# Optimization experiments

Measured on AMD Instinct MI355X. Metric: run time of the kernel, lower is better.

Reference implementation:

```python
import jax, jax.numpy as jnp
import numpy as np
import math

NUM_LEVELS = 16
LEVEL_DIM = 2
BASE_RES = 16
MAX_RES = 2048
HASHMAP_SIZE = 1 << 19  # 2**log2_hashmap_size
B, N = 4, 262144


def setup_inputs() -> dict:
    key = jax.random.key(0)
    k1, k2 = jax.random.split(key)
    x = jax.random.uniform(k1, (B, N, 3), dtype=jnp.float32)  # coords in [0,1]
    # per-level hash tables, init uniform(-1e-4, 1e-4) as in the torch module
    embeddings = jax.random.uniform(
        k2, (NUM_LEVELS, HASHMAP_SIZE, LEVEL_DIM),
        minval=-1e-4, maxval=1e-4, dtype=jnp.float32)
    return {"x": x, "embeddings": embeddings}


def reference(x, embeddings):
    # per_level_scale = exp((ln(max)-ln(base))/(L-1))
    per_level_scale = math.exp((math.log(MAX_RES) - math.log(BASE_RES)) / (NUM_LEVELS - 1))
    H = HASHMAP_SIZE
    feats = []
    for level in range(NUM_LEVELS):
        res = int(BASE_RES * per_level_scale ** level)  # static per level
        # floor coords, wrap into [0, res)
        cf = jnp.floor(x * res).astype(jnp.int32) % res  # [B,N,3]
        # hash = (c0 + c1*res + c2*res^2) mod H, computed in modular arithmetic
        # so everything fits in int32 (max term ~2047 * (2^19-1) < 2^31).
        h = (cf[..., 0] % H
             + (cf[..., 1] * res) % H
             + (cf[..., 2] * ((res * res) % H)) % H) % H  # [B,N]
        feats.append(embeddings[level][h])  # gather -> [B,N,LEVEL_DIM]
    return jnp.concatenate(feats, axis=-1)  # [B,N,NUM_LEVELS*LEVEL_DIM]
```

## Files before the change

### kernel.cpp

```cpp
#include <hip/hip_runtime.h>
#include <cmath>

#define NLEVELS 16
#define HSIZE   (1 << 19)
#define HMASK   (HSIZE - 1)

typedef float v2f __attribute__((ext_vector_type(2)));
typedef float v4f __attribute__((ext_vector_type(4)));

struct LevelParams {
    int res[NLEVELS];
    int r2mod[NLEVELS];
};

__device__ __forceinline__ int hash_one(float x0, float x1, float x2, int res, int r2)
{
    const float fr = (float)res;
    int c0 = (int)floorf(x0 * fr); if (c0 >= res) c0 -= res;
    int c1 = (int)floorf(x1 * fr); if (c1 >= res) c1 -= res;
    int c2 = (int)floorf(x2 * fr); if (c2 >= res) c2 -= res;
    return (c0 + ((c1 * res) & HMASK) + ((c2 * r2) & HMASK)) & HMASK;
}

__global__ __launch_bounds__(256)
void hashgrid_gather(const float* __restrict__ x,
                     const float* __restrict__ emb,
                     v2f* __restrict__ ws,
                     LevelParams lp, int npts)
{
    __shared__ float sx[256 * 3];

    const int tid   = threadIdx.x;
    const int g     = blockIdx.x & 7;
    const int chunk = blockIdx.x >> 3;
    const int block_base = chunk * 256;

    const int nfl   = npts * 3;
    const int base3 = block_base * 3;
    #pragma unroll
    for (int k = 0; k < 3; ++k) {
        int idx = base3 + tid + k * 256;
        if (idx < nfl) sx[tid + k * 256] = __builtin_nontemporal_load(&x[idx]);
    }
    __syncthreads();

    const int p = block_base + tid;
    if (p >= npts) return;

    const float x0 = sx[tid * 3 + 0];
    const float x1 = sx[tid * 3 + 1];
    const float x2 = sx[tid * 3 + 2];

    const v2f* __restrict__ e2 = (const v2f*)emb;

    const int lA = g;
    const int lB = 15 - g;

    const int hA = hash_one(x0, x1, x2, lp.res[lA], lp.r2mod[lA]);
    const int hB = hash_one(x0, x1, x2, lp.res[lB], lp.r2mod[lB]);

    const v2f vA = e2[(size_t)lA * HSIZE + hA];
    const v2f vB = e2[(size_t)lB * HSIZE + hB];

    __builtin_nontemporal_store(vA, &ws[(size_t)lA * npts + p]);
    __builtin_nontemporal_store(vB, &ws[(size_t)lB * npts + p]);
}

__global__ __launch_bounds__(256)
void hashgrid_transpose(const v2f* __restrict__ ws,
                        v4f* __restrict__ out4, int npts)
{
    const int t = blockIdx.x * 256 + threadIdx.x;
    const int p = t >> 3;
    const int j = t & 7;
    if (p >= npts) return;

    const v2f a = __builtin_nontemporal_load(&ws[(size_t)(2 * j)     * npts + p]);
    const v2f b = __builtin_nontemporal_load(&ws[(size_t)(2 * j + 1) * npts + p]);

    v4f o; o.x = a.x; o.y = a.y; o.z = b.x; o.w = b.y;
    __builtin_nontemporal_store(o, &out4[(size_t)p * 8 + j]);
}

__global__ __launch_bounds__(256)
void hashgrid_fwd(const float* __restrict__ x,
                  const float* __restrict__ emb,
                  float* __restrict__ out,
                  LevelParams lp, int npts)
{
    __shared__ float sx[256 * 3];
    const int tid        = threadIdx.x;
    const int block_base = blockIdx.x * 256;
    const int nfl        = npts * 3;
    const int base3      = block_base * 3;
    #pragma unroll
    for (int k = 0; k < 3; ++k) {
        int idx = base3 + tid + k * 256;
        if (idx < nfl) sx[tid + k * 256] = x[idx];
    }
    __syncthreads();
    const int p = block_base + tid;
    if (p >= npts) return;
    const float x0 = sx[tid * 3 + 0], x1 = sx[tid * 3 + 1], x2 = sx[tid * 3 + 2];
    const float2* __restrict__ e2 = (const float2*)emb;
    float2 v[NLEVELS];
    #pragma unroll
    for (int l = 0; l < NLEVELS; ++l) {
        const int h = hash_one(x0, x1, x2, lp.res[l], lp.r2mod[l]);
        v[l] = e2[(size_t)l * HSIZE + h];
    }
    float4* __restrict__ o4 = (float4*)(out + (size_t)p * (NLEVELS * 2));
    #pragma unroll
    for (int i = 0; i < 8; ++i)
        o4[i] = make_float4(v[2 * i].x, v[2 * i].y, v[2 * i + 1].x, v[2 * i + 1].y);
}

extern "C" void kernel_launch(void* const* d_in, const int* in_sizes, int n_in,
                              void* d_out, int out_size, void* d_ws, size_t ws_size,
                              hipStream_t stream)
{
    const float* x   = (const float*)d_in[0];
    const float* emb = (const float*)d_in[1];
    float*       out = (float*)d_out;

    const int npts = in_sizes[0] / 3;

    LevelParams lp;
    const double s = std::exp((std::log(2048.0) - std::log(16.0)) / 15.0);
    for (int l = 0; l < NLEVELS; ++l) {
        const double r = 16.0 * std::pow(s, (double)l);
        const int res  = (int)r;
        lp.res[l]   = res;
        lp.r2mod[l] = (int)(((long long)res * res) % HSIZE);
    }

    const size_t ws_need = (size_t)NLEVELS * (size_t)npts * sizeof(v2f);
    if (ws_size >= ws_need) {
        const int chunks  = (npts + 255) / 256;
        const int grid1   = chunks * 8;
        hipLaunchKernelGGL(hashgrid_gather, dim3(grid1), dim3(256), 0, stream,
                           x, emb, (v2f*)d_ws, lp, npts);
        const int grid2 = (npts * 8 + 255) / 256;
        hipLaunchKernelGGL(hashgrid_transpose, dim3(grid2), dim3(256), 0, stream,
                           (const v2f*)d_ws, (v4f*)out, npts);
    } else {
        const int blocks = (npts + 255) / 256;
        hipLaunchKernelGGL(hashgrid_fwd, dim3(blocks), dim3(256), 0, stream,
                           x, emb, out, lp, npts);
    }
}
```

Baseline: 371.3 us.

## Stage transpose through LDS and use nontemporal loads for high-res levels

The transpose kernel now has each block load all 16 level vectors for 256 points into padded shared memory, then write fully contiguous float4 rows of the output. The old version had each thread read two strided workspace entries. Separately, the gather kernel uses nontemporal loads for the larger-resolution levels (g>=5), which are assumed to have poor cache reuse, so they pollute the cache less. The costs are 34KB of LDS per block, which limits occupancy, and a barrier in the transpose.

```diff
diff --git a/kernel.cpp b/kernel.cpp
--- a/kernel.cpp
+++ b/kernel.cpp
@@ -59,7 +59,12 @@
     const int hA = hash_one(x0, x1, x2, lp.res[lA], lp.r2mod[lA]);
     const int hB = hash_one(x0, x1, x2, lp.res[lB], lp.r2mod[lB]);
 
-    const v2f vA = e2[(size_t)lA * HSIZE + hA];
+    v2f vA;
+    if (g >= 5) {
+        vA = __builtin_nontemporal_load(&e2[(size_t)lA * HSIZE + hA]);
+    } else {
+        vA = e2[(size_t)lA * HSIZE + hA];
+    }
     const v2f vB = e2[(size_t)lB * HSIZE + hB];
 
     __builtin_nontemporal_store(vA, &ws[(size_t)lA * npts + p]);
@@ -70,16 +75,43 @@
 void hashgrid_transpose(const v2f* __restrict__ ws,
                         v4f* __restrict__ out4, int npts)
 {
-    const int t = blockIdx.x * 256 + threadIdx.x;
-    const int p = t >> 3;
-    const int j = t & 7;
-    if (p >= npts) return;
+    __shared__ v2f s2[256][17];
 
-    const v2f a = __builtin_nontemporal_load(&ws[(size_t)(2 * j)     * npts + p]);
-    const v2f b = __builtin_nontemporal_load(&ws[(size_t)(2 * j + 1) * npts + p]);
+    const int tid = threadIdx.x;
+    const int block_base = blockIdx.x * 256;
+    const int p = block_base + tid;
 
-    v4f o; o.x = a.x; o.y = a.y; o.z = b.x; o.w = b.y;
-    __builtin_nontemporal_store(o, &out4[(size_t)p * 8 + j]);
+    if (p < npts) {
+        #pragma unroll
+        for (int l = 0; l < NLEVELS; ++l)
+            s2[tid][l] = ws[(size_t)l * npts + p];
+    }
+    __syncthreads();
+
+    if (block_base + 256 <= npts) {
+        #pragma unroll
+        for (int i = 0; i < 8; ++i) {
+            const int t  = i * 256 + tid;
+            const int q  = t >> 3;
+            const int j  = t & 7;
+            const v2f a = s2[q][2 * j];
+            const v2f b = s2[q][2 * j + 1];
+            v4f o; o.x = a.x; o.y = a.y; o.z = b.x; o.w = b.y;
+            __builtin_nontemporal_store(o, &out4[(size_t)block_base * 8 + t]);
+        }
+    } else {
+        for (int i = 0; i < 8; ++i) {
+            const int t = i * 256 + tid;
+            const int q = t >> 3;
+            if (block_base + q < npts) {
+                const int j = t & 7;
+                const v2f a = s2[q][2 * j];
+                const v2f b = s2[q][2 * j + 1];
+                v4f o; o.x = a.x; o.y = a.y; o.z = b.x; o.w = b.y;
+                __builtin_nontemporal_store(o, &out4[(size_t)block_base * 8 + t]);
+            }
+        }
+    }
 }
 
 __global__ __launch_bounds__(256)
@@ -136,12 +168,11 @@
 
     const size_t ws_need = (size_t)NLEVELS * (size_t)npts * sizeof(v2f);
     if (ws_size >= ws_need) {
-        const int chunks  = (npts + 255) / 256;
-        const int grid1   = chunks * 8;
-        hipLaunchKernelGGL(hashgrid_gather, dim3(grid1), dim3(256), 0, stream,
+        const int chunks = (npts + 255) / 256;
+        hipLaunchKernelGGL(hashgrid_gather, dim3(chunks * 8), dim3(256), 0, stream,
                            x, emb, (v2f*)d_ws, lp, npts);
-        const int grid2 = (npts * 8 + 255) / 256;
-        hipLaunchKernelGGL(hashgrid_transpose, dim3(grid2), dim3(256), 0, stream,
+        const int blocks2 = (npts + 255) / 256;
+        hipLaunchKernelGGL(hashgrid_transpose, dim3(blocks2), dim3(256), 0, stream,
                            (const v2f*)d_ws, (v4f*)out, npts);
     } else {
         const int blocks = (npts + 255) / 256;
```

Result: no change. 376.5 us (+1.4%).
